# Performance work log

Hardware: AMD Instinct MI355X
Metric: run time of the kernel (lower is better)

Reference implementation:

```python
import jax, jax.numpy as jnp
import numpy as np

EPSILON = 0.001  # binarization clip epsilon (both weights and inputs)
F32_EPS = float(np.finfo(np.float32).eps)

@jax.custom_jvp
def floor_ste(x):
    """Floor with straight-through-estimator gradient."""
    return jnp.floor(x)

@floor_ste.defjvp
def _floor_ste_jvp(primals, tangents):
    (x,), (t,) = primals, tangents
    return jnp.floor(x), t

def binarize(x, axis, epsilon):
    # bound = max-abs reduction over `axis`, kept dims; stop-gradient per original.
    bound = jax.lax.stop_gradient(
        jnp.max(jnp.abs(x), axis=axis, keepdims=True) + F32_EPS)
    scale = 1.0 / bound
    clip_bound = 1.0 - epsilon
    xq = jnp.clip(x * scale, -clip_bound, clip_bound)
    xq = floor_ste(xq) + 0.5  # maps (-inf,0)->-0.5, [0,inf)->+0.5 in scaled units
    return xq / scale

def setup_inputs() -> dict:
    key = jax.random.key(0)
    k1, k2 = jax.random.split(key)
    B, S, D, F = 4, 2048, 4096, 16384
    x = jax.random.normal(k1, (B, S, D), dtype=jnp.float32)
    # lecun_normal-style kernel init
    kernel = jax.random.normal(k2, (D, F), dtype=jnp.float32) / np.sqrt(D)
    bias = jnp.zeros((F,), dtype=jnp.float32)
    return {"x": x, "kernel": kernel, "bias": bias}

def reference(x, kernel, bias):
    # Binarize kernel per-output-feature (scale_axis 'auto' -> axis 0): bound (1, F)
    kq = binarize(kernel, (0,), EPSILON)
    # Binarize inputs per-token (scale_axis 'auto' -> axis 2): bound (B, S, 1)
    xq = binarize(x, (2,), EPSILON)
    # y[b,s,f] = sum_d xq[b,s,d] * kq[d,f]
    y = jnp.einsum('bsd,df->bsf', xq, kq)
    return y + bias[None, None, :]
```

## Files before the change

kernel.cpp:

```cpp
#include <hip/hip_runtime.h>
#include <stdint.h>


#define M_ROWS 8192
#define D_DIM  4096
#define F_DIM  16384
#define KW     128
#define F32_EPS 1.1920928955078125e-7f

typedef int v4i  __attribute__((ext_vector_type(4)));
typedef int v16i __attribute__((ext_vector_type(16)));

__global__ __launch_bounds__(256) void pack_x(const float* __restrict__ x,
                                              uint32_t* __restrict__ xbits,
                                              float2* __restrict__ bxs) {
    const int row  = blockIdx.x;
    const int tid  = threadIdx.x;
    const int lane = tid & 63;
    const int wv   = tid >> 6;
    const float* xr = x + (size_t)row * D_DIM;
    float mv = 0.f;
    int   pc = 0;
#pragma unroll
    for (int it = 0; it < 16; ++it) {
        float v = xr[it * 256 + tid];
        mv = fmaxf(mv, fabsf(v));
        unsigned long long m = __ballot(v >= 0.f);
        if (lane == 0) {
            pc += __popcll(m);
            uint2 wp = make_uint2((uint32_t)m, (uint32_t)(m >> 32));
            *(uint2*)&xbits[(size_t)row * KW + 2 * (it * 4 + wv)] = wp;
        }
    }
#pragma unroll
    for (int off = 32; off > 0; off >>= 1)
        mv = fmaxf(mv, __shfl_down(mv, off, 64));
    __shared__ float sm[4];
    __shared__ int   sp[4];
    if (lane == 0) { sm[wv] = mv; sp[wv] = pc; }
    __syncthreads();
    if (tid == 0) {
        float m4 = fmaxf(fmaxf(sm[0], sm[1]), fmaxf(sm[2], sm[3]));
        int   s  = sp[0] + sp[1] + sp[2] + sp[3];
        bxs[row] = make_float2(m4 + F32_EPS, (float)(D_DIM - 2 * s));
    }
}

__global__ __launch_bounds__(256) void pack_k(const float* __restrict__ kern,
                                              uint32_t* __restrict__ kbits,
                                              float* __restrict__ bkpart) {
    const int f   = blockIdx.x * 256 + threadIdx.x;
    const int seg = blockIdx.y;
    const int d0  = seg * 512;
    const float* kp = kern + (size_t)d0 * F_DIM + f;
    float mv = 0.f;
#pragma unroll 1
    for (int wq = 0; wq < 16; wq += 4) {
        uint32_t w4[4];
#pragma unroll
        for (int q = 0; q < 4; ++q) {
            uint32_t wrd = 0;
#pragma unroll
            for (int b = 0; b < 32; ++b) {
                float v = kp[(size_t)((wq + q) * 32 + b) * F_DIM];
                mv = fmaxf(mv, fabsf(v));
                wrd |= (v >= 0.f ? 1u : 0u) << b;
            }
            w4[q] = wrd;
        }
        *(uint4*)&kbits[(size_t)f * KW + seg * 16 + wq] =
            make_uint4(w4[0], w4[1], w4[2], w4[3]);
    }
    bkpart[seg * F_DIM + f] = mv;
}

__global__ __launch_bounds__(256) void reduce_bk(const float* __restrict__ bkpart,
                                                 const uint32_t* __restrict__ kbits,
                                                 float2* __restrict__ bks) {
    const int f = blockIdx.x * 256 + threadIdx.x;
    float m = 0.f;
#pragma unroll
    for (int seg = 0; seg < 8; ++seg)
        m = fmaxf(m, bkpart[seg * F_DIM + f]);
    int cnt = 0;
    const uint4* kr = (const uint4*)&kbits[(size_t)f * KW];
#pragma unroll
    for (int q = 0; q < 32; ++q) {
        uint4 v = kr[q];
        cnt += __popc(v.x) + __popc(v.y) + __popc(v.z) + __popc(v.w);
    }
    bks[f] = make_float2(0.25f * (m + F32_EPS), (float)(2 * cnt));
}

#define BM  128
#define BN  256
#define BKB 128
#define NIT (D_DIM / BKB)
#define SWZ(r, c) ((c) ^ (((r) & 7) << 4))

__device__ __forceinline__ uint4 expand16(uint32_t w, int sh) {
    uint4 r;
    r.x = (((w >> (sh +  0)) & 0xFu) * 0x00204081u) & 0x01010101u;
    r.y = (((w >> (sh +  4)) & 0xFu) * 0x00204081u) & 0x01010101u;
    r.z = (((w >> (sh +  8)) & 0xFu) * 0x00204081u) & 0x01010101u;
    r.w = (((w >> (sh + 12)) & 0xFu) * 0x00204081u) & 0x01010101u;
    return r;
}

__global__ __launch_bounds__(256, 2) void bgemm(const uint32_t* __restrict__ xbits,
                                                const uint32_t* __restrict__ kbits,
                                                const float2* __restrict__ bxs,
                                                const float2* __restrict__ bks,
                                                const float* __restrict__ bias,
                                                float* __restrict__ out) {
    __shared__ uint4 xs4[BM * BKB / 16];
    __shared__ uint4 ks4[BN * BKB / 16];
    uint8_t* xs = (uint8_t*)xs4;
    uint8_t* ks = (uint8_t*)ks4;

    const int tid = threadIdx.x;
    const int m0 = blockIdx.y * BM;
    const int n0 = blockIdx.x * BN;

    const int arow = tid >> 1;
    const int acb0 = (tid & 1) * 64;
    const uint32_t* gA = xbits + (size_t)(m0 + arow) * KW + (tid & 1) * 2;
    const uint32_t* gB = kbits + (size_t)(n0 + tid) * KW;
    uint2 ra = *(const uint2*)gA;
    uint4 rb = *(const uint4*)gB;

    const int lane = tid & 63;
    const int lo   = lane & 31;
    const int hi   = lane >> 5;
    const int wv   = tid >> 6;
    const int wm   = wv >> 1;
    const int wn   = wv & 1;
    const int arow0 = wm * 64 + lo;
    const int brow0 = wn * 128 + lo;
    const int swz   = (lo & 7) << 4;
    const int cshi  = hi * 16;

    v16i acc[2][4] = {};

    for (int it = 0; it < NIT; ++it) {
        {
            uint8_t* xd = xs + arow * BKB;
            *(uint4*)&xd[SWZ(arow, acb0 +  0)] = expand16(ra.x,  0);
            *(uint4*)&xd[SWZ(arow, acb0 + 16)] = expand16(ra.x, 16);
            *(uint4*)&xd[SWZ(arow, acb0 + 32)] = expand16(ra.y,  0);
            *(uint4*)&xd[SWZ(arow, acb0 + 48)] = expand16(ra.y, 16);
            uint8_t* kd = ks + tid * BKB;
            *(uint4*)&kd[SWZ(tid,   0)] = expand16(rb.x,  0);
            *(uint4*)&kd[SWZ(tid,  16)] = expand16(rb.x, 16);
            *(uint4*)&kd[SWZ(tid,  32)] = expand16(rb.y,  0);
            *(uint4*)&kd[SWZ(tid,  48)] = expand16(rb.y, 16);
            *(uint4*)&kd[SWZ(tid,  64)] = expand16(rb.z,  0);
            *(uint4*)&kd[SWZ(tid,  80)] = expand16(rb.z, 16);
            *(uint4*)&kd[SWZ(tid,  96)] = expand16(rb.w,  0);
            *(uint4*)&kd[SWZ(tid, 112)] = expand16(rb.w, 16);
        }
        if (it + 1 < NIT) {
            gA += 4; gB += 4;
            ra = *(const uint2*)gA;
            rb = *(const uint4*)gB;
        }
        __syncthreads();

#pragma unroll
        for (int kst = 0; kst < 4; ++kst) {
            const int cb = ((kst * 32) | cshi) ^ swz;
            v4i a[2], b[4];
#pragma unroll
            for (int i = 0; i < 2; ++i)
                a[i] = *(const v4i*)(xs + (arow0 + i * 32) * BKB + cb);
#pragma unroll
            for (int j = 0; j < 4; ++j)
                b[j] = *(const v4i*)(ks + (brow0 + j * 32) * BKB + cb);
#pragma unroll
            for (int i = 0; i < 2; ++i)
#pragma unroll
                for (int j = 0; j < 4; ++j)
                    acc[i][j] = __builtin_amdgcn_mfma_i32_32x32x32_i8(
                        a[i], b[j], acc[i][j], 0, 0, 0);
        }
        __syncthreads();
    }

    const int colb = n0 + wn * 128 + lo;
    float2 bkv[4]; float bz[4];
#pragma unroll
    for (int j = 0; j < 4; ++j) {
        bkv[j] = bks[colb + j * 32];
        bz[j]  = bias[colb + j * 32];
    }
    const int rowb = m0 + wm * 64 + 4 * hi;
#pragma unroll
    for (int i = 0; i < 2; ++i) {
#pragma unroll
        for (int rq = 0; rq < 4; ++rq) {
#pragma unroll
            for (int rr = 0; rr < 4; ++rr) {
                const int r   = rq * 4 + rr;
                const int row = rowb + i * 32 + 8 * rq + rr;
                const float2 bxv = bxs[row];
                float* orow = out + (size_t)row * F_DIM;
#pragma unroll
                for (int j = 0; j < 4; ++j) {
                    const float t = 4.f * (float)acc[i][j][r] + (bxv.y - bkv[j].y);
                    orow[colb + j * 32] = bxv.x * bkv[j].x * t + bz[j];
                }
            }
        }
    }
}

extern "C" void kernel_launch(void* const* d_in, const int* in_sizes, int n_in,
                              void* d_out, int out_size, void* d_ws, size_t ws_size,
                              hipStream_t stream) {
    const float* x    = (const float*)d_in[0];
    const float* kern = (const float*)d_in[1];
    const float* bias = (const float*)d_in[2];
    float* out = (float*)d_out;

    uint8_t* ws = (uint8_t*)d_ws;
    uint32_t* xbits  = (uint32_t*)ws;
    uint32_t* kbits  = (uint32_t*)(ws + 4194304);
    float2*   bxs    = (float2*)(ws + 12582912);
    float2*   bks    = (float2*)(ws + 12648448);
    float*    bkpart = (float*)(ws + 12779520);

    pack_x   <<<M_ROWS, 256, 0, stream>>>(x, xbits, bxs);
    pack_k   <<<dim3(64, 8), 256, 0, stream>>>(kern, kbits, bkpart);
    reduce_bk<<<64, 256, 0, stream>>>(bkpart, kbits, bks);
    bgemm    <<<dim3(F_DIM / BN, M_ROWS / BM), 256, 0, stream>>>(
                 xbits, kbits, bxs, bks, bias, out);
}
```

Before: 1.355 ms.

## Tile-major bit layout, double-buffered 256x256 binary GEMM, atomic kernel max

Repacks the x and kernel sign bits into a tile-major layout so each GEMM block reads coalesced 32-bit words per k-step. The GEMM moves to 256x256 tiles with 512 threads, a 64-deep k-step, a new swizzle and double-buffered LDS, so staging the next tile overlaps the MFMA work. It also raises wave priority around the MFMAs. pack_k now reads float4 across four features and reduces the per-feature max with atomicMax on the float bits, which needs a memset first. The risks are LDS and register pressure from the larger tile and the extra memset.

```diff
diff --git a/kernel.cpp b/kernel.cpp
--- a/kernel.cpp
+++ b/kernel.cpp
@@ -5,7 +5,7 @@
 #define M_ROWS 8192
 #define D_DIM  4096
 #define F_DIM  16384
-#define KW     128
+#define NKI    64
 #define F32_EPS 1.1920928955078125e-7f
 
 typedef int v4i  __attribute__((ext_vector_type(4)));
@@ -19,6 +19,7 @@
     const int lane = tid & 63;
     const int wv   = tid >> 6;
     const float* xr = x + (size_t)row * D_DIM;
+    uint32_t* xt = xbits + (size_t)(row >> 8) * (NKI * 512);
     float mv = 0.f;
     int   pc = 0;
 #pragma unroll
@@ -28,8 +29,9 @@
         unsigned long long m = __ballot(v >= 0.f);
         if (lane == 0) {
             pc += __popcll(m);
-            uint2 wp = make_uint2((uint32_t)m, (uint32_t)(m >> 32));
-            *(uint2*)&xbits[(size_t)row * KW + 2 * (it * 4 + wv)] = wp;
+            const int ki = it * 4 + wv;
+            *(uint2*)&xt[(size_t)ki * 512 + (row & 255) * 2] =
+                make_uint2((uint32_t)m, (uint32_t)(m >> 32));
         }
     }
 #pragma unroll
@@ -48,55 +50,55 @@
 
 __global__ __launch_bounds__(256) void pack_k(const float* __restrict__ kern,
                                               uint32_t* __restrict__ kbits,
-                                              float* __restrict__ bkpart) {
-    const int f   = blockIdx.x * 256 + threadIdx.x;
-    const int seg = blockIdx.y;
-    const int d0  = seg * 512;
-    const float* kp = kern + (size_t)d0 * F_DIM + f;
-    float mv = 0.f;
+                                              uint32_t* __restrict__ bkmax) {
+    const int tid = threadIdx.x;
+    const int f0  = blockIdx.x * 1024 + tid * 4;
+    const int d0  = blockIdx.y * 128;
+    const float* kp = kern + (size_t)d0 * F_DIM + f0;
+    uint32_t w[4][4] = {{0}};
+    float mx[4] = {0.f, 0.f, 0.f, 0.f};
 #pragma unroll 1
-    for (int wq = 0; wq < 16; wq += 4) {
-        uint32_t w4[4];
-#pragma unroll
-        for (int q = 0; q < 4; ++q) {
-            uint32_t wrd = 0;
-#pragma unroll
-            for (int b = 0; b < 32; ++b) {
-                float v = kp[(size_t)((wq + q) * 32 + b) * F_DIM];
-                mv = fmaxf(mv, fabsf(v));
-                wrd |= (v >= 0.f ? 1u : 0u) << b;
-            }
-            w4[q] = wrd;
-        }
-        *(uint4*)&kbits[(size_t)f * KW + seg * 16 + wq] =
-            make_uint4(w4[0], w4[1], w4[2], w4[3]);
-    }
-    bkpart[seg * F_DIM + f] = mv;
-}
-
-__global__ __launch_bounds__(256) void reduce_bk(const float* __restrict__ bkpart,
+    for (int dw = 0; dw < 4; ++dw) {
+#pragma unroll
+        for (int b = 0; b < 32; ++b) {
+            float4 v = *(const float4*)&kp[(size_t)(dw * 32 + b) * F_DIM];
+            mx[0] = fmaxf(mx[0], fabsf(v.x)); w[0][dw] |= (v.x >= 0.f ? 1u : 0u) << b;
+            mx[1] = fmaxf(mx[1], fabsf(v.y)); w[1][dw] |= (v.y >= 0.f ? 1u : 0u) << b;
+            mx[2] = fmaxf(mx[2], fabsf(v.z)); w[2][dw] |= (v.z >= 0.f ? 1u : 0u) << b;
+            mx[3] = fmaxf(mx[3], fabsf(v.w)); w[3][dw] |= (v.w >= 0.f ? 1u : 0u) << b;
+        }
+    }
+    uint32_t* kt = kbits + (size_t)(f0 >> 8) * (NKI * 512)
+                         + (size_t)(blockIdx.y * 2) * 512;
+#pragma unroll
+    for (int c = 0; c < 4; ++c) {
+        const int fo = ((f0 + c) & 255) * 2;
+        *(uint2*)&kt[fo]       = make_uint2(w[c][0], w[c][1]);
+        *(uint2*)&kt[512 + fo] = make_uint2(w[c][2], w[c][3]);
+        atomicMax(&bkmax[f0 + c], __float_as_uint(mx[c]));
+    }
+}
+
+__global__ __launch_bounds__(256) void reduce_bk(const uint32_t* __restrict__ bkmax,
                                                  const uint32_t* __restrict__ kbits,
                                                  float2* __restrict__ bks) {
     const int f = blockIdx.x * 256 + threadIdx.x;
-    float m = 0.f;
-#pragma unroll
-    for (int seg = 0; seg < 8; ++seg)
-        m = fmaxf(m, bkpart[seg * F_DIM + f]);
+    const uint32_t* kt = kbits + (size_t)(f >> 8) * (NKI * 512) + (f & 255) * 2;
     int cnt = 0;
-    const uint4* kr = (const uint4*)&kbits[(size_t)f * KW];
-#pragma unroll
-    for (int q = 0; q < 32; ++q) {
-        uint4 v = kr[q];
-        cnt += __popc(v.x) + __popc(v.y) + __popc(v.z) + __popc(v.w);
-    }
+#pragma unroll
+    for (int ki = 0; ki < NKI; ++ki) {
+        uint2 v = *(const uint2*)&kt[(size_t)ki * 512];
+        cnt += __popc(v.x) + __popc(v.y);
+    }
+    float m = __uint_as_float(bkmax[f]);
     bks[f] = make_float2(0.25f * (m + F32_EPS), (float)(2 * cnt));
 }
 
-#define BM  128
+#define BM  256
 #define BN  256
-#define BKB 128
+#define BKB 64
 #define NIT (D_DIM / BKB)
-#define SWZ(r, c) ((c) ^ (((r) & 7) << 4))
+#define SWZ64(r, c) ((c) ^ ((((r) >> 1) & 3) << 4))
 
 __device__ __forceinline__ uint4 expand16(uint32_t w, int sh) {
     uint4 r;
@@ -107,95 +109,95 @@
     return r;
 }
 
-__global__ __launch_bounds__(256, 2) void bgemm(const uint32_t* __restrict__ xbits,
+__global__ __launch_bounds__(512, 2) void bgemm(const uint32_t* __restrict__ xbits,
                                                 const uint32_t* __restrict__ kbits,
                                                 const float2* __restrict__ bxs,
                                                 const float2* __restrict__ bks,
                                                 const float* __restrict__ bias,
                                                 float* __restrict__ out) {
-    __shared__ uint4 xs4[BM * BKB / 16];
-    __shared__ uint4 ks4[BN * BKB / 16];
-    uint8_t* xs = (uint8_t*)xs4;
-    uint8_t* ks = (uint8_t*)ks4;
+    __shared__ uint4 xs4[2][BM * BKB / 16];
+    __shared__ uint4 ks4[2][BN * BKB / 16];
 
     const int tid = threadIdx.x;
     const int m0 = blockIdx.y * BM;
     const int n0 = blockIdx.x * BN;
 
-    const int arow = tid >> 1;
-    const int acb0 = (tid & 1) * 64;
-    const uint32_t* gA = xbits + (size_t)(m0 + arow) * KW + (tid & 1) * 2;
-    const uint32_t* gB = kbits + (size_t)(n0 + tid) * KW;
-    uint2 ra = *(const uint2*)gA;
-    uint4 rb = *(const uint4*)gB;
+    const uint32_t* gA = xbits + (size_t)blockIdx.y * (NKI * 512) + tid;
+    const uint32_t* gB = kbits + (size_t)blockIdx.x * (NKI * 512) + tid;
+
+    const int srow = tid >> 1;
+    const int sc0  = (tid & 1) * 32;
 
     const int lane = tid & 63;
     const int lo   = lane & 31;
     const int hi   = lane >> 5;
     const int wv   = tid >> 6;
-    const int wm   = wv >> 1;
-    const int wn   = wv & 1;
-    const int arow0 = wm * 64 + lo;
-    const int brow0 = wn * 128 + lo;
-    const int swz   = (lo & 7) << 4;
-    const int cshi  = hi * 16;
-
-    v16i acc[2][4] = {};
-
-    for (int it = 0; it < NIT; ++it) {
-        {
-            uint8_t* xd = xs + arow * BKB;
-            *(uint4*)&xd[SWZ(arow, acb0 +  0)] = expand16(ra.x,  0);
-            *(uint4*)&xd[SWZ(arow, acb0 + 16)] = expand16(ra.x, 16);
-            *(uint4*)&xd[SWZ(arow, acb0 + 32)] = expand16(ra.y,  0);
-            *(uint4*)&xd[SWZ(arow, acb0 + 48)] = expand16(ra.y, 16);
-            uint8_t* kd = ks + tid * BKB;
-            *(uint4*)&kd[SWZ(tid,   0)] = expand16(rb.x,  0);
-            *(uint4*)&kd[SWZ(tid,  16)] = expand16(rb.x, 16);
-            *(uint4*)&kd[SWZ(tid,  32)] = expand16(rb.y,  0);
-            *(uint4*)&kd[SWZ(tid,  48)] = expand16(rb.y, 16);
-            *(uint4*)&kd[SWZ(tid,  64)] = expand16(rb.z,  0);
-            *(uint4*)&kd[SWZ(tid,  80)] = expand16(rb.z, 16);
-            *(uint4*)&kd[SWZ(tid,  96)] = expand16(rb.w,  0);
-            *(uint4*)&kd[SWZ(tid, 112)] = expand16(rb.w, 16);
-        }
-        if (it + 1 < NIT) {
-            gA += 4; gB += 4;
-            ra = *(const uint2*)gA;
-            rb = *(const uint4*)gB;
-        }
-        __syncthreads();
-
-#pragma unroll
-        for (int kst = 0; kst < 4; ++kst) {
-            const int cb = ((kst * 32) | cshi) ^ swz;
-            v4i a[2], b[4];
-#pragma unroll
-            for (int i = 0; i < 2; ++i)
-                a[i] = *(const v4i*)(xs + (arow0 + i * 32) * BKB + cb);
-#pragma unroll
-            for (int j = 0; j < 4; ++j)
-                b[j] = *(const v4i*)(ks + (brow0 + j * 32) * BKB + cb);
-#pragma unroll
-            for (int i = 0; i < 2; ++i)
-#pragma unroll
-                for (int j = 0; j < 4; ++j)
+    const int wm   = wv >> 2;
+    const int wn   = wv & 3;
+    const int swz  = ((lo >> 1) & 3) << 4;
+    const int cshi = hi * 16;
+
+    v16i acc[4][2] = {};
+
+    uint32_t wa = gA[0], wb = gB[0];
+
+    auto STAGE = [&](int buf, uint32_t A, uint32_t B) {
+        uint8_t* xd = (uint8_t*)xs4[buf] + srow * BKB;
+        *(uint4*)&xd[SWZ64(srow, sc0)]      = expand16(A, 0);
+        *(uint4*)&xd[SWZ64(srow, sc0 + 16)] = expand16(A, 16);
+        uint8_t* kd = (uint8_t*)ks4[buf] + srow * BKB;
+        *(uint4*)&kd[SWZ64(srow, sc0)]      = expand16(B, 0);
+        *(uint4*)&kd[SWZ64(srow, sc0 + 16)] = expand16(B, 16);
+    };
+
+    STAGE(0, wa, wb);
+    wa = gA[512]; wb = gB[512];
+    __syncthreads();
+
+#pragma unroll 2
+    for (int t = 0; t < NIT; ++t) {
+        const int cur = t & 1;
+        if (t + 1 < NIT) {
+            STAGE(cur ^ 1, wa, wb);
+            if (t + 2 < NIT) {
+                wa = gA[(size_t)(t + 2) * 512];
+                wb = gB[(size_t)(t + 2) * 512];
+            }
+        }
+        const uint8_t* xb = (const uint8_t*)xs4[cur];
+        const uint8_t* kb = (const uint8_t*)ks4[cur];
+        __builtin_amdgcn_s_setprio(1);
+#pragma unroll
+        for (int kst = 0; kst < 2; ++kst) {
+            const int cb = (kst * 32 + cshi) ^ swz;
+            v4i a[4], b[2];
+#pragma unroll
+            for (int i = 0; i < 4; ++i)
+                a[i] = *(const v4i*)(xb + (wm * 128 + lo + i * 32) * BKB + cb);
+#pragma unroll
+            for (int j = 0; j < 2; ++j)
+                b[j] = *(const v4i*)(kb + (wn * 64 + lo + j * 32) * BKB + cb);
+#pragma unroll
+            for (int i = 0; i < 4; ++i)
+#pragma unroll
+                for (int j = 0; j < 2; ++j)
                     acc[i][j] = __builtin_amdgcn_mfma_i32_32x32x32_i8(
                         a[i], b[j], acc[i][j], 0, 0, 0);
         }
+        __builtin_amdgcn_s_setprio(0);
         __syncthreads();
     }
 
-    const int colb = n0 + wn * 128 + lo;
-    float2 bkv[4]; float bz[4];
-#pragma unroll
-    for (int j = 0; j < 4; ++j) {
+    const int colb = n0 + wn * 64 + lo;
+    float2 bkv[2]; float bz[2];
+#pragma unroll
+    for (int j = 0; j < 2; ++j) {
         bkv[j] = bks[colb + j * 32];
         bz[j]  = bias[colb + j * 32];
     }
-    const int rowb = m0 + wm * 64 + 4 * hi;
-#pragma unroll
-    for (int i = 0; i < 2; ++i) {
+    const int rowb = m0 + wm * 128 + 4 * hi;
+#pragma unroll
+    for (int i = 0; i < 4; ++i) {
 #pragma unroll
         for (int rq = 0; rq < 4; ++rq) {
 #pragma unroll
@@ -205,9 +207,9 @@
                 const float2 bxv = bxs[row];
                 float* orow = out + (size_t)row * F_DIM;
 #pragma unroll
-                for (int j = 0; j < 4; ++j) {
-                    const float t = 4.f * (float)acc[i][j][r] + (bxv.y - bkv[j].y);
-                    orow[colb + j * 32] = bxv.x * bkv[j].x * t + bz[j];
+                for (int j = 0; j < 2; ++j) {
+                    const float tv = 4.f * (float)acc[i][j][r] + (bxv.y - bkv[j].y);
+                    orow[colb + j * 32] = bxv.x * bkv[j].x * tv + bz[j];
                 }
             }
         }
@@ -223,15 +225,16 @@
     float* out = (float*)d_out;
 
     uint8_t* ws = (uint8_t*)d_ws;
-    uint32_t* xbits  = (uint32_t*)ws;
-    uint32_t* kbits  = (uint32_t*)(ws + 4194304);
-    float2*   bxs    = (float2*)(ws + 12582912);
-    float2*   bks    = (float2*)(ws + 12648448);
-    float*    bkpart = (float*)(ws + 12779520);
-
+    uint32_t* xbits = (uint32_t*)ws;
+    uint32_t* kbits = (uint32_t*)(ws + 4194304);
+    float2*   bxs   = (float2*)(ws + 12582912);
+    float2*   bks   = (float2*)(ws + 12648448);
+    uint32_t* bkmax = (uint32_t*)(ws + 12779520);
+
+    hipMemsetAsync(bkmax, 0, 65536, stream);
     pack_x   <<<M_ROWS, 256, 0, stream>>>(x, xbits, bxs);
-    pack_k   <<<dim3(64, 8), 256, 0, stream>>>(kern, kbits, bkpart);
-    reduce_bk<<<64, 256, 0, stream>>>(bkpart, kbits, bks);
-    bgemm    <<<dim3(F_DIM / BN, M_ROWS / BM), 256, 0, stream>>>(
+    pack_k   <<<dim3(16, 32), 256, 0, stream>>>(kern, kbits, bkmax);
+    reduce_bk<<<64, 256, 0, stream>>>(bkmax, kbits, bks);
+    bgemm    <<<dim3(F_DIM / BN, M_ROWS / BM), 512, 0, stream>>>(
                  xbits, kbits, bxs, bks, bias, out);
 }
```

Result: faster. 1.231 ms (-9.1%).
